# Optimization experiments

Measured on AMD Instinct MI355X. Metric: run time of the kernel, lower is better.

## Reference

```python
import jax, jax.numpy as jnp
import numpy as np

N_NODES = 50000
N_HEDGES = 10000
NNZ = 200000
OBS = 128
LAT = 256
N_STEPS = 8  # fixed-step RK4 steps over [0, 1]


def setup_inputs() -> dict:
    key = jax.random.key(0)
    ks = jax.random.split(key, 16)

    def lin(k, fan_in, fan_out):
        return jax.random.normal(k, (fan_in, fan_out), jnp.float32) / np.float32(np.sqrt(fan_in))

    return {
        "node_features": jax.random.normal(ks[0], (N_NODES, OBS), jnp.float32),
        "enc_W0": lin(ks[1], OBS, LAT), "enc_b0": jnp.zeros((LAT,), jnp.float32),
        "enc_W1": lin(ks[2], LAT, LAT), "enc_b1": jnp.zeros((LAT,), jnp.float32),
        "conv_Wne": lin(ks[3], LAT, LAT), "conv_bne": jnp.zeros((LAT,), jnp.float32),
        "conv_Wen": lin(ks[4], LAT, LAT), "conv_ben": jnp.zeros((LAT,), jnp.float32),
        "dec_W0": lin(ks[5], LAT, LAT), "dec_b0": jnp.zeros((LAT,), jnp.float32),
        "dec_W1": lin(ks[6], LAT, OBS), "dec_b1": jnp.zeros((OBS,), jnp.float32),
        "node_idx": jax.random.randint(ks[7], (NNZ,), 0, N_NODES),
        "edge_idx": jax.random.randint(ks[8], (NNZ,), 0, N_HEDGES),
    }


def reference(node_features, enc_W0, enc_b0, enc_W1, enc_b1,
              conv_Wne, conv_bne, conv_Wen, conv_ben,
              dec_W0, dec_b0, dec_W1, dec_b1,
              node_idx, edge_idx):
    ones = jnp.ones((NNZ,), jnp.float32)
    edge_cnt = jnp.clip(jax.ops.segment_sum(ones, edge_idx, N_HEDGES), 1.0)[:, None]
    node_cnt = jnp.clip(jax.ops.segment_sum(ones, node_idx, N_NODES), 1.0)[:, None]

    def conv(z):  # z: [n, LAT]
        # node -> hyperedge: mean-aggregate incident node states, then transform
        e = jax.ops.segment_sum(z[node_idx], edge_idx, N_HEDGES) / edge_cnt  # [m, LAT]
        e = e @ conv_Wne + conv_bne
        # hyperedge -> node: mean-aggregate incident edge states, then transform
        m = jax.ops.segment_sum(e[edge_idx], node_idx, N_NODES) / node_cnt   # [n, LAT]
        return m @ conv_Wen + conv_ben

    def f(z):  # ODE vector field: dz/dt = tanh(conv(z))
        return jnp.tanh(conv(z))

    # encode (MLP depth=1: linear -> relu -> linear)
    z0 = jax.nn.relu(node_features @ enc_W0 + enc_b0) @ enc_W1 + enc_b1

    dt = jnp.float32(1.0 / N_STEPS)  # integrate t0=0 -> t1=1

    def rk4_step(z, _):
        k1 = f(z)
        k2 = f(z + 0.5 * dt * k1)
        k3 = f(z + 0.5 * dt * k2)
        k4 = f(z + dt * k3)
        return z + (dt / 6.0) * (k1 + 2.0 * k2 + 2.0 * k3 + k4), None

    z1, _ = jax.lax.scan(rk4_step, z0, None, length=N_STEPS)

    # decode
    return jax.nn.relu(z1 @ dec_W0 + dec_b0) @ dec_W1 + dec_b1
```

## Files before the change

kernel.cpp:

```cpp
#include <hip/hip_runtime.h>

#define NN 50000
#define NE 10000
#define NNZC 200000
#define OBSD 128
#define LATD 256
#define NSTEPS 8

typedef unsigned short u16;
typedef unsigned char u8;
typedef __attribute__((ext_vector_type(8))) short bf16x8;
typedef __attribute__((ext_vector_type(4))) float f32x4;
typedef __attribute__((ext_vector_type(2))) float f32x2;
typedef __attribute__((ext_vector_type(4))) u16 us4;
typedef __attribute__((ext_vector_type(8))) u16 us8;
typedef __attribute__((ext_vector_type(16))) u16 us16;
typedef __attribute__((ext_vector_type(2))) unsigned int u32x2;
typedef __attribute__((ext_vector_type(4))) unsigned int u32x4;

__device__ __forceinline__ u16 f2b(float f) {
  unsigned int u = __builtin_bit_cast(unsigned int, f);
  u = (u + 0x7FFFu + ((u >> 16) & 1u)) >> 16;
  return (u16)u;
}
__device__ __forceinline__ float b2f(u16 h) {
  unsigned int u = ((unsigned int)h) << 16;
  return __builtin_bit_cast(float, u);
}
__device__ __forceinline__ float fast_tanh(float x) {
  float e = __expf(2.0f * x);
  return 1.0f - 2.0f / (e + 1.0f);
}

__device__ __forceinline__ void fp8_dec4(unsigned int w, float* o) {
  f32x2 a = __builtin_amdgcn_cvt_pk_f32_fp8((int)w, false);
  f32x2 b = __builtin_amdgcn_cvt_pk_f32_fp8((int)w, true);
  o[0] = a[0]; o[1] = a[1]; o[2] = b[0]; o[3] = b[1];
}
__device__ __forceinline__ void fp8_dec16(u32x4 w, float* o) {
#pragma unroll
  for (int q = 0; q < 4; ++q) fp8_dec4(w[q], o + q * 4);
}
__device__ __forceinline__ unsigned int fp8_enc4(const float* v) {
  int lo = __builtin_amdgcn_cvt_pk_fp8_f32(v[0], v[1], 0, false);
  lo = __builtin_amdgcn_cvt_pk_fp8_f32(v[2], v[3], lo, true);
  return (unsigned int)lo;
}

typedef __attribute__((address_space(1))) const unsigned int GU32;
typedef __attribute__((address_space(3))) unsigned int LU32;
__device__ __forceinline__ void async16(const void* g, void* l) {
  __builtin_amdgcn_global_load_lds((GU32*)g, (LU32*)l, 16, 0, 0);
}


__global__ void count_kernel(const int* __restrict__ ni, const int* __restrict__ ei,
                             int* __restrict__ cnt_n, int* __restrict__ cnt_e, int nnz) {
  int i = blockIdx.x * blockDim.x + threadIdx.x;
  if (i < nnz) {
    atomicAdd(&cnt_n[ni[i]], 1);
    atomicAdd(&cnt_e[ei[i]], 1);
  }
}

__global__ __launch_bounds__(1024) void scan1_kernel(
    const int* __restrict__ cnt_e, int* __restrict__ off_e, int* __restrict__ bsum_e, int ne, int nbe,
    const int* __restrict__ cnt_n, int* __restrict__ off_n, int* __restrict__ bsum_n, int nn) {
  __shared__ int ws[16];
  const int b = blockIdx.x;
  const int* cnt; int* off; int* bsum; int n, bi;
  if (b < nbe) { cnt = cnt_e; off = off_e; bsum = bsum_e; n = ne; bi = b; }
  else         { cnt = cnt_n; off = off_n; bsum = bsum_n; n = nn; bi = b - nbe; }
  const int tid = threadIdx.x;
  const int lane = tid & 63, w = tid >> 6;
  const int i = bi * 1024 + tid;
  int v = (i < n) ? cnt[i] : 0;
  int s = v;
#pragma unroll
  for (int d = 1; d < 64; d <<= 1) {
    int t2 = __shfl_up(s, d);
    if (lane >= d) s += t2;
  }
  if (lane == 63) ws[w] = s;
  __syncthreads();
  if (w == 0) {
    int x = (lane < 16) ? ws[lane] : 0;
#pragma unroll
    for (int d = 1; d < 16; d <<= 1) {
      int t2 = __shfl_up(x, d);
      if (lane >= d) x += t2;
    }
    if (lane < 16) ws[lane] = x;
  }
  __syncthreads();
  const int base = w ? ws[w - 1] : 0;
  if (i < n) off[i] = base + s - v;
  if (tid == 0) bsum[bi] = ws[15];
}

__global__ void scan2_kernel(int* __restrict__ bsum_e, int nbe,
                             int* __restrict__ bsum_n, int nbn) {
  int* bsum = (threadIdx.x < 64) ? bsum_e : bsum_n;
  const int nb = (threadIdx.x < 64) ? nbe : nbn;
  const int lane = threadIdx.x & 63;
  int v = (lane < nb) ? bsum[lane] : 0;
  int s = v;
#pragma unroll
  for (int d = 1; d < 64; d <<= 1) {
    int t2 = __shfl_up(s, d);
    if (lane >= d) s += t2;
  }
  if (lane < nb) bsum[lane] = s - v;
  if (lane == 63) bsum[nb] = s;
}

__global__ void scan3_kernel(
    const int* __restrict__ cnt_e, int* __restrict__ off_e, int* __restrict__ cur_e,
    float* __restrict__ recip_e, const int* __restrict__ bsum_e, int ne,
    const int* __restrict__ cnt_n, int* __restrict__ off_n, int* __restrict__ cur_n,
    float* __restrict__ recip_n, const int* __restrict__ bsum_n, int nn) {
  const int* cnt; int* off; int* cur; float* recip; const int* bsum; int n;
  if (blockIdx.y == 0) { cnt = cnt_e; off = off_e; cur = cur_e; recip = recip_e; bsum = bsum_e; n = ne; }
  else                 { cnt = cnt_n; off = off_n; cur = cur_n; recip = recip_n; bsum = bsum_n; n = nn; }
  const int i = blockIdx.x * blockDim.x + threadIdx.x;
  if (i < n) {
    const int o = off[i] + bsum[i >> 10];
    off[i] = o;
    cur[i] = o;
    recip[i] = 1.0f / fmaxf((float)cnt[i], 1.0f);
  }
  if (i == 0) off[n] = bsum[(n + 1023) >> 10];
}

__global__ void fill_kernel(const int* __restrict__ ni, const int* __restrict__ ei,
                            int* __restrict__ cur_n, int* __restrict__ cur_e,
                            int* __restrict__ lst_n, int* __restrict__ lst_e, int nnz) {
  int i = blockIdx.x * blockDim.x + threadIdx.x;
  if (i < nnz) {
    int n = ni[i], e = ei[i];
    lst_e[atomicAdd(&cur_e[e], 1)] = n;
    lst_n[atomicAdd(&cur_n[n], 1)] = e;
  }
}


__global__ void prep_kernel(const float* __restrict__ encW0, const float* __restrict__ encW1,
                            const float* __restrict__ Wen, const float* __restrict__ decW0,
                            const float* __restrict__ decW1, const float* __restrict__ Wne,
                            u16* __restrict__ encW0T, u16* __restrict__ encW1T,
                            u16* __restrict__ WenT, u16* __restrict__ decW0T,
                            u16* __restrict__ decW1T, u16* __restrict__ WneB) {
  const int job = blockIdx.y;
  const int i = blockIdx.x * 256 + threadIdx.x;
  const float* src; u16* dst; int K = LATD, N = LATD; bool tr = true;
  switch (job) {
    case 0: src = encW0; dst = encW0T; K = OBSD; break;
    case 1: src = encW1; dst = encW1T; break;
    case 2: src = Wen;   dst = WenT;   break;
    case 3: src = decW0; dst = decW0T; break;
    case 4: src = decW1; dst = decW1T; N = OBSD; break;
    default: src = Wne;  dst = WneB;   tr = false; break;
  }
  if (i >= K * N) return;
  if (tr) {
    const int k = i / N, n = i - k * N;
    dst[n * K + k] = f2b(src[i]);
  } else {
    dst[i] = f2b(src[i]);
  }
}

__global__ void to_bf16_kernel(const float* __restrict__ src, u16* __restrict__ dst, int n) {
  int i = (blockIdx.x * blockDim.x + threadIdx.x) * 4;
  if (i >= n) return;
  float4 v = *reinterpret_cast<const float4*>(src + i);
  us4 o;
  o.x = f2b(v.x); o.y = f2b(v.y); o.z = f2b(v.z); o.w = f2b(v.w);
  *reinterpret_cast<us4*>(dst + i) = o;
}

__global__ void dvec_kernel(const float* __restrict__ bne, const float* __restrict__ Wen,
                            const float* __restrict__ ben, float* __restrict__ d) {
  const int j = threadIdx.x;
  float s = ben[j];
  for (int k = 0; k < LATD; ++k) s += bne[k] * Wen[k * LATD + j];
  d[j] = s;
}


template <int FP8SRC>
__global__ __launch_bounds__(256) void agg_kernel(const void* __restrict__ src,
                                                  const int* __restrict__ off,
                                                  const int* __restrict__ lst,
                                                  const float* __restrict__ recip,
                                                  u16* __restrict__ dst, int nseg) {
  constexpr int GW = FP8SRC ? 16 : 32;
  constexpr int EPL = LATD / GW;
  const int t = threadIdx.x;
  const int gl = t & (GW - 1);
  const int seg = blockIdx.x * (256 / GW) + (t / GW);
  if (seg >= nseg) return;
  const int s = off[seg], e = off[seg + 1];
  float a[EPL] = {};
  int p = s;
  if constexpr (FP8SRC) {
    for (; p + 8 <= e; p += 8) {
      u32x4 w[8];
#pragma unroll
      for (int q = 0; q < 8; ++q)
        w[q] = *(const u32x4*)((const u8*)src + (size_t)lst[p + q] * LATD + gl * 16);
#pragma unroll
      for (int q = 0; q < 8; ++q) {
        float f[16];
        fp8_dec16(w[q], f);
#pragma unroll
        for (int j = 0; j < 16; ++j) a[j] += f[j];
      }
    }
    for (; p + 4 <= e; p += 4) {
      u32x4 w[4];
#pragma unroll
      for (int q = 0; q < 4; ++q)
        w[q] = *(const u32x4*)((const u8*)src + (size_t)lst[p + q] * LATD + gl * 16);
#pragma unroll
      for (int q = 0; q < 4; ++q) {
        float f[16];
        fp8_dec16(w[q], f);
#pragma unroll
        for (int j = 0; j < 16; ++j) a[j] += f[j];
      }
    }
    for (; p < e; ++p) {
      const u32x4 w = *(const u32x4*)((const u8*)src + (size_t)lst[p] * LATD + gl * 16);
      float f[16];
      fp8_dec16(w, f);
#pragma unroll
      for (int j = 0; j < 16; ++j) a[j] += f[j];
    }
  } else {
    for (; p + 8 <= e; p += 8) {
      us8 v[8];
#pragma unroll
      for (int q = 0; q < 8; ++q)
        v[q] = *(const us8*)((const u16*)src + (size_t)lst[p + q] * LATD + gl * 8);
#pragma unroll
      for (int q = 0; q < 8; ++q)
#pragma unroll
        for (int j = 0; j < 8; ++j) a[j] += b2f(v[q][j]);
    }
    for (; p + 4 <= e; p += 4) {
      us8 v[4];
#pragma unroll
      for (int q = 0; q < 4; ++q)
        v[q] = *(const us8*)((const u16*)src + (size_t)lst[p + q] * LATD + gl * 8);
#pragma unroll
      for (int q = 0; q < 4; ++q)
#pragma unroll
        for (int j = 0; j < 8; ++j) a[j] += b2f(v[q][j]);
    }
    for (; p < e; ++p) {
      const us8 v = *(const us8*)((const u16*)src + (size_t)lst[p] * LATD + gl * 8);
#pragma unroll
      for (int j = 0; j < 8; ++j) a[j] += b2f(v[j]);
    }
  }
  const float rc = recip[seg];
  const size_t base = (size_t)seg * LATD + gl * EPL;
  if constexpr (FP8SRC) {
    us16 o;
#pragma unroll
    for (int j = 0; j < 16; ++j) o[j] = f2b(a[j] * rc);
    *(us16*)(dst + base) = o;
  } else {
    us8 o;
#pragma unroll
    for (int j = 0; j < 8; ++j) o[j] = f2b(a[j] * rc);
    *(us8*)(dst + base) = o;
  }
}


template <int STAGE>
__global__ __launch_bounds__(256) void aggn_epi_kernel(
    const void* __restrict__ G, const int* __restrict__ off, const int* __restrict__ lst,
    const float* __restrict__ recip, const float* __restrict__ dvec,
    u16* __restrict__ ub, const u8* __restrict__ k2s, const u8* __restrict__ k3s,
    u8* __restrict__ kout8, u16* __restrict__ zhi, float c) {
  constexpr int GW = (STAGE == 0) ? 32 : 16;
  constexpr int EPL = LATD / GW;
  const int t = threadIdx.x;
  const int gl = t & (GW - 1);
  const int node = blockIdx.x * (256 / GW) + (t / GW);
  if (node >= NN) return;
  const int s = off[node], e = off[node + 1];
  float v[EPL] = {};
  int p = s;
  if constexpr (STAGE == 0) {
    for (; p + 4 <= e; p += 4) {
      us8 g[4];
#pragma unroll
      for (int q = 0; q < 4; ++q)
        g[q] = *(const us8*)((const u16*)G + (size_t)lst[p + q] * LATD + gl * 8);
#pragma unroll
      for (int q = 0; q < 4; ++q)
#pragma unroll
        for (int j = 0; j < 8; ++j) v[j] += b2f(g[q][j]);
    }
    for (; p < e; ++p) {
      const us8 g = *(const us8*)((const u16*)G + (size_t)lst[p] * LATD + gl * 8);
#pragma unroll
      for (int j = 0; j < 8; ++j) v[j] += b2f(g[j]);
    }
  } else {
    for (; p + 4 <= e; p += 4) {
      u32x4 w[4];
#pragma unroll
      for (int q = 0; q < 4; ++q)
        w[q] = *(const u32x4*)((const u8*)G + (size_t)lst[p + q] * LATD + gl * 16);
#pragma unroll
      for (int q = 0; q < 4; ++q) {
        float f[16];
        fp8_dec16(w[q], f);
#pragma unroll
        for (int j = 0; j < 16; ++j) v[j] += f[j];
      }
    }
    for (; p < e; ++p) {
      const u32x4 w = *(const u32x4*)((const u8*)G + (size_t)lst[p] * LATD + gl * 16);
      float f[16];
      fp8_dec16(w, f);
#pragma unroll
      for (int j = 0; j < 16; ++j) v[j] += f[j];
    }
  }
  const float rc = recip[node];
  const size_t base = (size_t)node * LATD + gl * EPL;
  const float dt6 = 0.125f / 6.0f;

  if constexpr (STAGE == 0) {
    float kv[8];
    us8 uo;
#pragma unroll
    for (int j = 0; j < 8; ++j) {
      const float u = v[j] * rc + dvec[gl * 8 + j];
      uo[j] = f2b(u);
      kv[j] = fast_tanh(u);
    }
    *(us8*)(ub + base) = uo;
    u32x2 kp;
    kp[0] = fp8_enc4(kv);
    kp[1] = fp8_enc4(kv + 4);
    *(u32x2*)(kout8 + base) = kp;
  } else if constexpr (STAGE == 1) {
    const us16 uv = *(const us16*)(ub + base);
    float kv[16];
#pragma unroll
    for (int j = 0; j < 16; ++j)
      kv[j] = fast_tanh(b2f(uv[j]) + c * (v[j] * rc));
    u32x4 kp;
#pragma unroll
    for (int q = 0; q < 4; ++q) kp[q] = fp8_enc4(kv + q * 4);
    *(u32x4*)(kout8 + base) = kp;
  } else {
    const us16 uv = *(const us16*)(ub + base);
    const u32x4 w2 = *(const u32x4*)(k2s + base);
    const u32x4 w3 = *(const u32x4*)(k3s + base);
    const us16 zh = *(const us16*)(zhi + base);
    float f2[16], f3[16];
    fp8_dec16(w2, f2);
    fp8_dec16(w3, f3);
    us16 ho;
#pragma unroll
    for (int j = 0; j < 16; ++j) {
      const float u = b2f(uv[j]);
      const float k1 = fast_tanh(u);
      const float k4 = fast_tanh(u + c * (v[j] * rc));
      const float zn = b2f(zh[j]) + dt6 * (k1 + 2.0f * f2[j] + 2.0f * f3[j] + k4);
      ho[j] = f2b(zn);
    }
    *(us16*)(zhi + base) = ho;
  }
}


template <int OUT8>
__global__ __launch_bounds__(256) void gemm64_kernel(
    const u16* __restrict__ A, const u16* __restrict__ BT,
    u16* __restrict__ Gb, u8* __restrict__ Gf8) {
  __shared__ char smem[4 * 16 * 66 * 4];
  u16* lA = (u16*)smem;
  u16* lB = (u16*)(smem + 4096);
  const int t = threadIdx.x;
  const int m0 = blockIdx.x * 64, n0 = blockIdx.y * 128;
  const int srow = t >> 2;
  const int gslot = (t & 3) ^ ((srow >> 1) & 3);

  int ar = m0 + srow; if (ar > NE - 1) ar = NE - 1;
  const u16* gA = A + (size_t)ar * LATD + gslot * 8;
  const u16* gB0 = BT + (size_t)(n0 + srow) * LATD + gslot * 8;
  const u16* gB1 = BT + (size_t)(n0 + 64 + srow) * LATD + gslot * 8;
  char* lAd = (char*)lA + t * 16;
  char* lBd0 = (char*)lB + t * 16;
  char* lBd1 = lBd0 + 4096;

  const int lane = t & 63, wid = t >> 6;
  const int lrow = lane & 15, kg = lane >> 4;

  f32x4 acc[4][2] = {};
  const char* lAb = (const char*)lA;
  const char* lBb = (const char*)lB;

  for (int c = 0; c < 8; ++c) {
    const int kk = c * 32;
    async16(gA + kk, lAd);
    async16(gB0 + kk, lBd0);
    async16(gB1 + kk, lBd1);
    __syncthreads();
    bf16x8 af[4], bg[2];
#pragma unroll
    for (int i = 0; i < 4; ++i) {
      const int rA = i * 16 + lrow;
      af[i] = *(const bf16x8*)(lAb + rA * 64 + (((kg ^ (rA >> 1)) & 3) << 4));
    }
#pragma unroll
    for (int j = 0; j < 2; ++j) {
      const int rB = wid * 32 + j * 16 + lrow;
      bg[j] = *(const bf16x8*)(lBb + rB * 64 + (((kg ^ (rB >> 1)) & 3) << 4));
    }
#pragma unroll
    for (int i = 0; i < 4; ++i)
#pragma unroll
      for (int j = 0; j < 2; ++j)
        acc[i][j] = __builtin_amdgcn_mfma_f32_16x16x32_bf16(af[i], bg[j], acc[i][j], 0, 0, 0);
    __syncthreads();
  }

  float* stage = (float*)smem + wid * (16 * 66);
  const int rr = lane >> 2;
  const int c0 = (lane & 3) * 8;

#pragma unroll
  for (int ti = 0; ti < 4; ++ti) {
#pragma unroll
    for (int tj = 0; tj < 2; ++tj)
#pragma unroll
      for (int j = 0; j < 4; ++j)
        stage[(kg * 4 + j) * 66 + tj * 16 + lrow] = acc[ti][tj][j];
    const int gr = m0 + ti * 16 + rr;
    if (gr < NE) {
      const int gc = n0 + wid * 32 + c0;
      const size_t idx = (size_t)gr * LATD + gc;
      float v[8];
      *(float4*)v = *(const float4*)&stage[rr * 66 + c0];
      *(float4*)(v + 4) = *(const float4*)&stage[rr * 66 + c0 + 4];
      if constexpr (OUT8) {
        u32x2 kp;
        kp[0] = fp8_enc4(v);
        kp[1] = fp8_enc4(v + 4);
        *(u32x2*)(Gf8 + idx) = kp;
      } else {
        us8 o;
#pragma unroll
        for (int e2 = 0; e2 < 8; ++e2) o[e2] = f2b(v[e2]);
        *(us8*)(Gb + idx) = o;
      }
    }
  }
}


enum { EPI_RELU_BF16, EPI_BF16, EPI_F32 };

template <int MODE>
__global__ __launch_bounds__(256) void gemm_kernel(
    const u16* __restrict__ A, const u16* __restrict__ BT, const float* __restrict__ bias,
    int M, int N, int K,
    u16* __restrict__ outb, float* __restrict__ outf) {
  __shared__ char smem[4 * 16 * 66 * 4];
  u16* lA = (u16*)smem;
  u16* lB = (u16*)(smem + 8192);
  const int t = threadIdx.x;
  const int m0 = blockIdx.x * 128, n0 = blockIdx.y * 128;
  const int srow = t >> 2;
  const int gslot = (t & 3) ^ ((srow >> 1) & 3);

  int ar0 = m0 + srow;      if (ar0 > M - 1) ar0 = M - 1;
  int ar1 = m0 + srow + 64; if (ar1 > M - 1) ar1 = M - 1;
  const u16* gA0 = A + (size_t)ar0 * K + gslot * 8;
  const u16* gA1 = A + (size_t)ar1 * K + gslot * 8;
  const u16* gB0 = BT + (size_t)(n0 + srow) * K + gslot * 8;
  const u16* gB1 = BT + (size_t)(n0 + srow + 64) * K + gslot * 8;
  char* lAd0 = (char*)lA + t * 16; char* lAd1 = lAd0 + 4096;
  char* lBd0 = (char*)lB + t * 16; char* lBd1 = lBd0 + 4096;

  const int lane = t & 63, wid = t >> 6;
  const int wm = wid >> 1, wn = wid & 1;
  const int lrow = lane & 15, kg = lane >> 4;

  f32x4 acc[4][4] = {};
  const char* lAb = (const char*)lA;
  const char* lBb = (const char*)lB;

  for (int kk = 0; kk < K; kk += 32) {
    async16(gA0 + kk, lAd0);
    async16(gA1 + kk, lAd1);
    async16(gB0 + kk, lBd0);
    async16(gB1 + kk, lBd1);
    __syncthreads();
    bf16x8 af[4], bg[4];
#pragma unroll
    for (int i = 0; i < 4; ++i) {
      int rA = wm * 64 + i * 16 + lrow;
      af[i] = *(const bf16x8*)(lAb + rA * 64 + (((kg ^ (rA >> 1)) & 3) << 4));
      int rB = wn * 64 + i * 16 + lrow;
      bg[i] = *(const bf16x8*)(lBb + rB * 64 + (((kg ^ (rB >> 1)) & 3) << 4));
    }
#pragma unroll
    for (int i = 0; i < 4; ++i)
#pragma unroll
      for (int j = 0; j < 4; ++j)
        acc[i][j] = __builtin_amdgcn_mfma_f32_16x16x32_bf16(af[i], bg[j], acc[i][j], 0, 0, 0);
    __syncthreads();
  }

  float* stage = (float*)smem + wid * (16 * 66);
  const int rr = lane >> 3;
  const int c0 = (lane & 7) * 8;

#pragma unroll
  for (int ti = 0; ti < 4; ++ti) {
#pragma unroll
    for (int tj = 0; tj < 4; ++tj) {
      const float bv = bias[n0 + wn * 64 + tj * 16 + lrow];
#pragma unroll
      for (int j = 0; j < 4; ++j)
        stage[(kg * 4 + j) * 66 + tj * 16 + lrow] = acc[ti][tj][j] + bv;
    }
#pragma unroll
    for (int pass = 0; pass < 2; ++pass) {
      const int r = pass * 8 + rr;
      const int gr = m0 + wm * 64 + ti * 16 + r;
      if (gr >= M) continue;
      const int gc = n0 + wn * 64 + c0;
      const size_t idx = (size_t)gr * N + gc;
      float v[8];
      *(float4*)v = *(const float4*)&stage[r * 66 + c0];
      *(float4*)(v + 4) = *(const float4*)&stage[r * 66 + c0 + 4];

      if constexpr (MODE == EPI_RELU_BF16 || MODE == EPI_BF16) {
        us8 o;
#pragma unroll
        for (int e2 = 0; e2 < 8; ++e2)
          o[e2] = f2b(MODE == EPI_RELU_BF16 ? fmaxf(v[e2], 0.0f) : v[e2]);
        *(us8*)(outb + idx) = o;
      } else {
        *(float4*)(outf + idx) = *(float4*)v;
        *(float4*)(outf + idx + 4) = *(float4*)(v + 4);
      }
    }
  }
}


extern "C" void kernel_launch(void* const* d_in, const int* in_sizes, int n_in,
                              void* d_out, int out_size, void* d_ws, size_t ws_size,
                              hipStream_t stream) {
  const float* X = (const float*)d_in[0];
  const float* encW0 = (const float*)d_in[1];
  const float* encb0 = (const float*)d_in[2];
  const float* encW1 = (const float*)d_in[3];
  const float* encb1 = (const float*)d_in[4];
  const float* Wne = (const float*)d_in[5];
  const float* bne = (const float*)d_in[6];
  const float* Wen = (const float*)d_in[7];
  const float* ben = (const float*)d_in[8];
  const float* decW0 = (const float*)d_in[9];
  const float* decb0 = (const float*)d_in[10];
  const float* decW1 = (const float*)d_in[11];
  const float* decb1 = (const float*)d_in[12];
  const int* node_idx = (const int*)d_in[13];
  const int* edge_idx = (const int*)d_in[14];
  float* out = (float*)d_out;

  char* p = (char*)d_ws;
  auto alloc = [&](size_t bytes) {
    char* r = p;
    p += (bytes + 255) & ~(size_t)255;
    return r;
  };
  u16* zhi      = (u16*)alloc((size_t)NN * LATD * 2);
  u16* ub       = (u16*)alloc((size_t)NN * LATD * 2);
  u16* h1b      = (u16*)alloc((size_t)NN * LATD * 2);
  u8*  pA       = (u8*)alloc((size_t)NN * LATD);
  u8*  pB       = (u8*)alloc((size_t)NN * LATD);
  u16* eagg     = (u16*)alloc((size_t)NE * LATD * 2);
  u16* Gb       = (u16*)alloc((size_t)NE * LATD * 2);
  u8*  Gf8      = (u8*)alloc((size_t)NE * LATD);
  u16* encW0T   = (u16*)alloc((size_t)OBSD * LATD * 2);
  u16* encW1T   = (u16*)alloc((size_t)LATD * LATD * 2);
  u16* WneB     = (u16*)alloc((size_t)LATD * LATD * 2);
  u16* WenT     = (u16*)alloc((size_t)LATD * LATD * 2);
  u16* WcT      = (u16*)alloc((size_t)LATD * LATD * 2);
  u16* decW0T   = (u16*)alloc((size_t)LATD * LATD * 2);
  u16* decW1T   = (u16*)alloc((size_t)LATD * OBSD * 2);
  float* dvec   = (float*)alloc(LATD * 4);
  float* zeros  = (float*)alloc(LATD * 4);
  int* cnt      = (int*)alloc((size_t)(NE + NN) * 4);
  int* cnt_e = cnt; int* cnt_n = cnt + NE;
  int* off_e    = (int*)alloc((size_t)(NE + 1) * 4);
  int* off_n    = (int*)alloc((size_t)(NN + 1) * 4);
  int* cur_e    = (int*)alloc((size_t)NE * 4);
  int* cur_n    = (int*)alloc((size_t)NN * 4);
  int* lst_e    = (int*)alloc((size_t)NNZC * 4);
  int* lst_n    = (int*)alloc((size_t)NNZC * 4);
  float* recip_e = (float*)alloc((size_t)NE * 4);
  float* recip_n = (float*)alloc((size_t)NN * 4);
  int* bsum_e   = (int*)alloc(16 * 4);
  int* bsum_n   = (int*)alloc(64 * 4);

  size_t needed = (size_t)(p - (char*)d_ws);
  if (needed > ws_size) {
    hipMemsetAsync(d_out, 0x7F, (size_t)out_size * 4, stream);
    return;
  }

  const int nbe = (NE + 1023) / 1024, nbn = (NN + 1023) / 1024;

  hipMemsetAsync(cnt, 0, (size_t)(NE + NN) * 4, stream);
  count_kernel<<<(NNZC + 255) / 256, 256, 0, stream>>>(node_idx, edge_idx, cnt_n, cnt_e, NNZC);
  scan1_kernel<<<nbe + nbn, 1024, 0, stream>>>(cnt_e, off_e, bsum_e, NE, nbe,
                                               cnt_n, off_n, bsum_n, NN);
  scan2_kernel<<<1, 128, 0, stream>>>(bsum_e, nbe, bsum_n, nbn);
  scan3_kernel<<<dim3((NN + 255) / 256, 2), 256, 0, stream>>>(
      cnt_e, off_e, cur_e, recip_e, bsum_e, NE,
      cnt_n, off_n, cur_n, recip_n, bsum_n, NN);
  fill_kernel<<<(NNZC + 255) / 256, 256, 0, stream>>>(node_idx, edge_idx, cur_n, cur_e, lst_n, lst_e, NNZC);

  prep_kernel<<<dim3(256, 6), 256, 0, stream>>>(encW0, encW1, Wen, decW0, decW1, Wne,
                                                encW0T, encW1T, WenT, decW0T, decW1T, WneB);
  hipMemsetAsync(zeros, 0, LATD * 4, stream);
  dvec_kernel<<<1, LATD, 0, stream>>>(bne, Wen, ben, dvec);
  gemm_kernel<EPI_BF16><<<dim3(2, 2), 256, 0, stream>>>(WenT, WneB, zeros, LATD, LATD, LATD,
                                                        WcT, nullptr);

  const dim3 blk(256);
  const dim3 g50((NN + 127) / 128, LATD / 128);
  const dim3 gdec((NN + 127) / 128, OBSD / 128);
  const dim3 g64((NE + 63) / 64, 2);
  const dim3 gae32((NE + 7) / 8);
  const dim3 gae16((NE + 15) / 16);
  const dim3 gan32((NN + 7) / 8);
  const dim3 gan16((NN + 15) / 16);

  to_bf16_kernel<<<(NN * OBSD / 4 + 255) / 256, 256, 0, stream>>>(X, (u16*)pA, NN * OBSD);
  gemm_kernel<EPI_RELU_BF16><<<g50, blk, 0, stream>>>((u16*)pA, encW0T, encb0, NN, LATD, OBSD,
                                                      h1b, nullptr);
  gemm_kernel<EPI_BF16><<<g50, blk, 0, stream>>>(h1b, encW1T, encb1, NN, LATD, LATD,
                                                 zhi, nullptr);

  for (int s = 0; s < NSTEPS; ++s) {
    agg_kernel<0><<<gae32, blk, 0, stream>>>(zhi, off_e, lst_e, recip_e, eagg, NE);
    gemm64_kernel<0><<<g64, blk, 0, stream>>>(eagg, WcT, Gb, nullptr);
    aggn_epi_kernel<0><<<gan32, blk, 0, stream>>>(Gb, off_n, lst_n, recip_n, dvec,
                                                  ub, nullptr, nullptr, pA, zhi, 0.f);
    agg_kernel<1><<<gae16, blk, 0, stream>>>(pA, off_e, lst_e, recip_e, eagg, NE);
    gemm64_kernel<1><<<g64, blk, 0, stream>>>(eagg, WcT, nullptr, Gf8);
    aggn_epi_kernel<1><<<gan16, blk, 0, stream>>>(Gf8, off_n, lst_n, recip_n, dvec,
                                                  ub, nullptr, nullptr, pB, zhi, 0.0625f);
    agg_kernel<1><<<gae16, blk, 0, stream>>>(pB, off_e, lst_e, recip_e, eagg, NE);
    gemm64_kernel<1><<<g64, blk, 0, stream>>>(eagg, WcT, nullptr, Gf8);
    aggn_epi_kernel<1><<<gan16, blk, 0, stream>>>(Gf8, off_n, lst_n, recip_n, dvec,
                                                  ub, nullptr, nullptr, pA, zhi, 0.0625f);
    agg_kernel<1><<<gae16, blk, 0, stream>>>(pA, off_e, lst_e, recip_e, eagg, NE);
    gemm64_kernel<1><<<g64, blk, 0, stream>>>(eagg, WcT, nullptr, Gf8);
    aggn_epi_kernel<3><<<gan16, blk, 0, stream>>>(Gf8, off_n, lst_n, recip_n, dvec,
                                                  ub, pB, pA, nullptr, zhi, 0.125f);
  }

  gemm_kernel<EPI_RELU_BF16><<<g50, blk, 0, stream>>>(zhi, decW0T, decb0, NN, LATD, LATD,
                                                      h1b, nullptr);
  gemm_kernel<EPI_F32><<<gdec, blk, 0, stream>>>(h1b, decW1T, decb1, NN, OBSD, LATD,
                                                 nullptr, out);
}
```

Measured before the change: 1.525 ms.

## Use fp8 G for the first RK stage, fold dvec into prep, drop 8-wide unroll

The first RK4 stage now writes its per-hyperedge GEMM output as fp8 instead of bf16, so the node-side gather reads half the bytes, and all aggn stages share a single 16-lane fp8 path. The separate dvec kernel is folded into prep_kernel as an extra grid row, removing one launch. The 8-wide unrolled gather loops in agg_kernel are removed, leaving only the 4-wide loop. Using fp8 in stage 0 lowers the precision of the G values feeding z updates, which adds accuracy risk, and the smaller unroll may reduce memory-level parallelism.

```diff
diff --git a/kernel.cpp b/kernel.cpp
--- a/kernel.cpp
+++ b/kernel.cpp
@@ -147,11 +147,22 @@
 __global__ void prep_kernel(const float* __restrict__ encW0, const float* __restrict__ encW1,
                             const float* __restrict__ Wen, const float* __restrict__ decW0,
                             const float* __restrict__ decW1, const float* __restrict__ Wne,
+                            const float* __restrict__ bne, const float* __restrict__ ben,
                             u16* __restrict__ encW0T, u16* __restrict__ encW1T,
                             u16* __restrict__ WenT, u16* __restrict__ decW0T,
-                            u16* __restrict__ decW1T, u16* __restrict__ WneB) {
+                            u16* __restrict__ decW1T, u16* __restrict__ WneB,
+                            float* __restrict__ dvec) {
   const int job = blockIdx.y;
   const int i = blockIdx.x * 256 + threadIdx.x;
+  if (job == 6) {
+    if (blockIdx.x == 0) {
+      const int j = threadIdx.x;
+      float s = ben[j];
+      for (int k = 0; k < LATD; ++k) s += bne[k] * Wen[k * LATD + j];
+      dvec[j] = s;
+    }
+    return;
+  }
   const float* src; u16* dst; int K = LATD, N = LATD; bool tr = true;
   switch (job) {
     case 0: src = encW0; dst = encW0T; K = OBSD; break;
@@ -177,14 +188,6 @@
   us4 o;
   o.x = f2b(v.x); o.y = f2b(v.y); o.z = f2b(v.z); o.w = f2b(v.w);
   *reinterpret_cast<us4*>(dst + i) = o;
-}
-
-__global__ void dvec_kernel(const float* __restrict__ bne, const float* __restrict__ Wen,
-                            const float* __restrict__ ben, float* __restrict__ d) {
-  const int j = threadIdx.x;
-  float s = ben[j];
-  for (int k = 0; k < LATD; ++k) s += bne[k] * Wen[k * LATD + j];
-  d[j] = s;
 }
 
 
@@ -204,19 +207,6 @@
   float a[EPL] = {};
   int p = s;
   if constexpr (FP8SRC) {
-    for (; p + 8 <= e; p += 8) {
-      u32x4 w[8];
-#pragma unroll
-      for (int q = 0; q < 8; ++q)
-        w[q] = *(const u32x4*)((const u8*)src + (size_t)lst[p + q] * LATD + gl * 16);
-#pragma unroll
-      for (int q = 0; q < 8; ++q) {
-        float f[16];
-        fp8_dec16(w[q], f);
-#pragma unroll
-        for (int j = 0; j < 16; ++j) a[j] += f[j];
-      }
-    }
     for (; p + 4 <= e; p += 4) {
       u32x4 w[4];
 #pragma unroll
@@ -238,16 +228,6 @@
       for (int j = 0; j < 16; ++j) a[j] += f[j];
     }
   } else {
-    for (; p + 8 <= e; p += 8) {
-      us8 v[8];
-#pragma unroll
-      for (int q = 0; q < 8; ++q)
-        v[q] = *(const us8*)((const u16*)src + (size_t)lst[p + q] * LATD + gl * 8);
-#pragma unroll
-      for (int q = 0; q < 8; ++q)
-#pragma unroll
-        for (int j = 0; j < 8; ++j) a[j] += b2f(v[q][j]);
-    }
     for (; p + 4 <= e; p += 4) {
       us8 v[4];
 #pragma unroll
@@ -282,75 +262,55 @@
 
 template <int STAGE>
 __global__ __launch_bounds__(256) void aggn_epi_kernel(
-    const void* __restrict__ G, const int* __restrict__ off, const int* __restrict__ lst,
+    const u8* __restrict__ G, const int* __restrict__ off, const int* __restrict__ lst,
     const float* __restrict__ recip, const float* __restrict__ dvec,
     u16* __restrict__ ub, const u8* __restrict__ k2s, const u8* __restrict__ k3s,
     u8* __restrict__ kout8, u16* __restrict__ zhi, float c) {
-  constexpr int GW = (STAGE == 0) ? 32 : 16;
-  constexpr int EPL = LATD / GW;
   const int t = threadIdx.x;
-  const int gl = t & (GW - 1);
-  const int node = blockIdx.x * (256 / GW) + (t / GW);
+  const int gl = t & 15;
+  const int node = blockIdx.x * 16 + (t >> 4);
   if (node >= NN) return;
   const int s = off[node], e = off[node + 1];
-  float v[EPL] = {};
+  float v[16] = {};
   int p = s;
+  for (; p + 4 <= e; p += 4) {
+    u32x4 w[4];
+#pragma unroll
+    for (int q = 0; q < 4; ++q)
+      w[q] = *(const u32x4*)(G + (size_t)lst[p + q] * LATD + gl * 16);
+#pragma unroll
+    for (int q = 0; q < 4; ++q) {
+      float f[16];
+      fp8_dec16(w[q], f);
+#pragma unroll
+      for (int j = 0; j < 16; ++j) v[j] += f[j];
+    }
+  }
+  for (; p < e; ++p) {
+    const u32x4 w = *(const u32x4*)(G + (size_t)lst[p] * LATD + gl * 16);
+    float f[16];
+    fp8_dec16(w, f);
+#pragma unroll
+    for (int j = 0; j < 16; ++j) v[j] += f[j];
+  }
+  const float rc = recip[node];
+  const size_t base = (size_t)node * LATD + gl * 16;
+  const float dt6 = 0.125f / 6.0f;
+
   if constexpr (STAGE == 0) {
-    for (; p + 4 <= e; p += 4) {
-      us8 g[4];
-#pragma unroll
-      for (int q = 0; q < 4; ++q)
-        g[q] = *(const us8*)((const u16*)G + (size_t)lst[p + q] * LATD + gl * 8);
-#pragma unroll
-      for (int q = 0; q < 4; ++q)
-#pragma unroll
-        for (int j = 0; j < 8; ++j) v[j] += b2f(g[q][j]);
-    }
-    for (; p < e; ++p) {
-      const us8 g = *(const us8*)((const u16*)G + (size_t)lst[p] * LATD + gl * 8);
-#pragma unroll
-      for (int j = 0; j < 8; ++j) v[j] += b2f(g[j]);
-    }
-  } else {
-    for (; p + 4 <= e; p += 4) {
-      u32x4 w[4];
-#pragma unroll
-      for (int q = 0; q < 4; ++q)
-        w[q] = *(const u32x4*)((const u8*)G + (size_t)lst[p + q] * LATD + gl * 16);
-#pragma unroll
-      for (int q = 0; q < 4; ++q) {
-        float f[16];
-        fp8_dec16(w[q], f);
-#pragma unroll
-        for (int j = 0; j < 16; ++j) v[j] += f[j];
-      }
-    }
-    for (; p < e; ++p) {
-      const u32x4 w = *(const u32x4*)((const u8*)G + (size_t)lst[p] * LATD + gl * 16);
-      float f[16];
-      fp8_dec16(w, f);
-#pragma unroll
-      for (int j = 0; j < 16; ++j) v[j] += f[j];
-    }
-  }
-  const float rc = recip[node];
-  const size_t base = (size_t)node * LATD + gl * EPL;
-  const float dt6 = 0.125f / 6.0f;
-
-  if constexpr (STAGE == 0) {
-    float kv[8];
-    us8 uo;
-#pragma unroll
-    for (int j = 0; j < 8; ++j) {
-      const float u = v[j] * rc + dvec[gl * 8 + j];
+    float kv[16];
+    us16 uo;
+#pragma unroll
+    for (int j = 0; j < 16; ++j) {
+      const float u = v[j] * rc + dvec[gl * 16 + j];
       uo[j] = f2b(u);
       kv[j] = fast_tanh(u);
     }
-    *(us8*)(ub + base) = uo;
-    u32x2 kp;
-    kp[0] = fp8_enc4(kv);
-    kp[1] = fp8_enc4(kv + 4);
-    *(u32x2*)(kout8 + base) = kp;
+    *(us16*)(ub + base) = uo;
+    u32x4 kp;
+#pragma unroll
+    for (int q = 0; q < 4; ++q) kp[q] = fp8_enc4(kv + q * 4);
+    *(u32x4*)(kout8 + base) = kp;
   } else if constexpr (STAGE == 1) {
     const us16 uv = *(const us16*)(ub + base);
     float kv[16];
@@ -383,10 +343,8 @@
 }
 
 
-template <int OUT8>
 __global__ __launch_bounds__(256) void gemm64_kernel(
-    const u16* __restrict__ A, const u16* __restrict__ BT,
-    u16* __restrict__ Gb, u8* __restrict__ Gf8) {
+    const u16* __restrict__ A, const u16* __restrict__ BT, u8* __restrict__ Gf8) {
   __shared__ char smem[4 * 16 * 66 * 4];
   u16* lA = (u16*)smem;
   u16* lB = (u16*)(smem + 4096);
@@ -453,17 +411,10 @@
       float v[8];
       *(float4*)v = *(const float4*)&stage[rr * 66 + c0];
       *(float4*)(v + 4) = *(const float4*)&stage[rr * 66 + c0 + 4];
-      if constexpr (OUT8) {
-        u32x2 kp;
-        kp[0] = fp8_enc4(v);
-        kp[1] = fp8_enc4(v + 4);
-        *(u32x2*)(Gf8 + idx) = kp;
-      } else {
-        us8 o;
-#pragma unroll
-        for (int e2 = 0; e2 < 8; ++e2) o[e2] = f2b(v[e2]);
-        *(us8*)(Gb + idx) = o;
-      }
+      u32x2 kp;
+      kp[0] = fp8_enc4(v);
+      kp[1] = fp8_enc4(v + 4);
+      *(u32x2*)(Gf8 + idx) = kp;
     }
   }
 }
@@ -594,7 +545,6 @@
   u8*  pA       = (u8*)alloc((size_t)NN * LATD);
   u8*  pB       = (u8*)alloc((size_t)NN * LATD);
   u16* eagg     = (u16*)alloc((size_t)NE * LATD * 2);
-  u16* Gb       = (u16*)alloc((size_t)NE * LATD * 2);
   u8*  Gf8      = (u8*)alloc((size_t)NE * LATD);
   u16* encW0T   = (u16*)alloc((size_t)OBSD * LATD * 2);
   u16* encW1T   = (u16*)alloc((size_t)LATD * LATD * 2);
@@ -636,10 +586,9 @@
       cnt_n, off_n, cur_n, recip_n, bsum_n, NN);
   fill_kernel<<<(NNZC + 255) / 256, 256, 0, stream>>>(node_idx, edge_idx, cur_n, cur_e, lst_n, lst_e, NNZC);
 
-  prep_kernel<<<dim3(256, 6), 256, 0, stream>>>(encW0, encW1, Wen, decW0, decW1, Wne,
-                                                encW0T, encW1T, WenT, decW0T, decW1T, WneB);
+  prep_kernel<<<dim3(256, 7), 256, 0, stream>>>(encW0, encW1, Wen, decW0, decW1, Wne, bne, ben,
+                                                encW0T, encW1T, WenT, decW0T, decW1T, WneB, dvec);
   hipMemsetAsync(zeros, 0, LATD * 4, stream);
-  dvec_kernel<<<1, LATD, 0, stream>>>(bne, Wen, ben, dvec);
   gemm_kernel<EPI_BF16><<<dim3(2, 2), 256, 0, stream>>>(WenT, WneB, zeros, LATD, LATD, LATD,
                                                         WcT, nullptr);
 
@@ -649,7 +598,6 @@
   const dim3 g64((NE + 63) / 64, 2);
   const dim3 gae32((NE + 7) / 8);
   const dim3 gae16((NE + 15) / 16);
-  const dim3 gan32((NN + 7) / 8);
   const dim3 gan16((NN + 15) / 16);
 
   to_bf16_kernel<<<(NN * OBSD / 4 + 255) / 256, 256, 0, stream>>>(X, (u16*)pA, NN * OBSD);
@@ -660,19 +608,19 @@
 
   for (int s = 0; s < NSTEPS; ++s) {
     agg_kernel<0><<<gae32, blk, 0, stream>>>(zhi, off_e, lst_e, recip_e, eagg, NE);
-    gemm64_kernel<0><<<g64, blk, 0, stream>>>(eagg, WcT, Gb, nullptr);
-    aggn_epi_kernel<0><<<gan32, blk, 0, stream>>>(Gb, off_n, lst_n, recip_n, dvec,
+    gemm64_kernel<<<g64, blk, 0, stream>>>(eagg, WcT, Gf8);
+    aggn_epi_kernel<0><<<gan16, blk, 0, stream>>>(Gf8, off_n, lst_n, recip_n, dvec,
                                                   ub, nullptr, nullptr, pA, zhi, 0.f);
     agg_kernel<1><<<gae16, blk, 0, stream>>>(pA, off_e, lst_e, recip_e, eagg, NE);
-    gemm64_kernel<1><<<g64, blk, 0, stream>>>(eagg, WcT, nullptr, Gf8);
+    gemm64_kernel<<<g64, blk, 0, stream>>>(eagg, WcT, Gf8);
     aggn_epi_kernel<1><<<gan16, blk, 0, stream>>>(Gf8, off_n, lst_n, recip_n, dvec,
                                                   ub, nullptr, nullptr, pB, zhi, 0.0625f);
     agg_kernel<1><<<gae16, blk, 0, stream>>>(pB, off_e, lst_e, recip_e, eagg, NE);
-    gemm64_kernel<1><<<g64, blk, 0, stream>>>(eagg, WcT, nullptr, Gf8);
+    gemm64_kernel<<<g64, blk, 0, stream>>>(eagg, WcT, Gf8);
     aggn_epi_kernel<1><<<gan16, blk, 0, stream>>>(Gf8, off_n, lst_n, recip_n, dvec,
                                                   ub, nullptr, nullptr, pA, zhi, 0.0625f);
     agg_kernel<1><<<gae16, blk, 0, stream>>>(pA, off_e, lst_e, recip_e, eagg, NE);
-    gemm64_kernel<1><<<g64, blk, 0, stream>>>(eagg, WcT, nullptr, Gf8);
+    gemm64_kernel<<<g64, blk, 0, stream>>>(eagg, WcT, Gf8);
     aggn_epi_kernel<3><<<gan16, blk, 0, stream>>>(Gf8, off_n, lst_n, recip_n, dvec,
                                                   ub, pB, pA, nullptr, zhi, 0.125f);
   }
```

New measurement: 1.532 ms. About the same (+0.5%).
